# Kernel tuning notes

Hardware: AMD Instinct MI355X
Metric: run time of the kernel (lower is better)

The kernel has to match this reference:

```python
import jax, jax.numpy as jnp
import numpy as np

B, S, E, H = 2, 2048, 512, 8
DH = E // H
SCALE = DH ** -0.5
TEMPERATURE = 1.0
LN_EPS = 1e-5


def setup_inputs() -> dict:
    key = jax.random.key(0)
    ks = jax.random.split(key, 12)
    s = E ** -0.5
    return {
        "q": jax.random.normal(ks[0], (B, S, E), jnp.float32),
        "k": jax.random.normal(ks[1], (B, S, E), jnp.float32),
        "v": jax.random.normal(ks[2], (B, S, E), jnp.float32),
        "Wq": jax.random.normal(ks[3], (E, E), jnp.float32) * s,
        "bq": jnp.zeros((E,), jnp.float32),
        "Wk": jax.random.normal(ks[4], (E, E), jnp.float32) * s,
        "bk": jnp.zeros((E,), jnp.float32),
        "Wv": jax.random.normal(ks[5], (E, E), jnp.float32) * s,
        "bv": jnp.zeros((E,), jnp.float32),
        "Wo": jax.random.normal(ks[6], (E, E), jnp.float32) * s,
        "bo": jnp.zeros((E,), jnp.float32),
        "ln_g": jnp.ones((E,), jnp.float32),
        "ln_b": jnp.zeros((E,), jnp.float32),
    }


def reference(q, k, v, Wq, bq, Wk, bk, Wv, bv, Wo, bo, ln_g, ln_b):
    # QKV projections (nn.Linear: x @ W.T + b)
    qh = (q @ Wq.T + bq).reshape(B, S, H, DH).transpose(0, 2, 1, 3)  # [B,H,S,Dh]
    kh = (k @ Wk.T + bk).reshape(B, S, H, DH).transpose(0, 2, 1, 3)
    vh = (v @ Wv.T + bv).reshape(B, S, H, DH).transpose(0, 2, 1, 3)
    # attention scores [B,H,S,S], scaled then divided by temperature
    scores = jnp.einsum('bhqd,bhkd->bhqk', qh, kh) * (SCALE / TEMPERATURE)
    attn = jax.nn.softmax(scores, axis=-1)
    # dropout is identity in eval mode
    x = jnp.einsum('bhqk,bhkd->bhqd', attn, vh)  # [B,H,S,Dh]
    x = x.transpose(0, 2, 1, 3).reshape(B, S, E)
    # out projection + LayerNorm
    y = x @ Wo.T + bo
    mu = jnp.mean(y, axis=-1, keepdims=True)
    var = jnp.var(y, axis=-1, keepdims=True)
    out = (y - mu) * jax.lax.rsqrt(var + LN_EPS) * ln_g + ln_b
    return out
```

## Files before the change

### kernel.cpp

```cpp
#include <hip/hip_runtime.h>
#include <hip/hip_bf16.h>
#include <stdint.h>

#define B_ 2
#define S_ 2048
#define E_ 512
#define H_ 8
#define DH_ 64
#define BH_ (B_*H_)
#define M_ (B_*S_)

typedef short short8 __attribute__((ext_vector_type(8)));
typedef float f32x4 __attribute__((ext_vector_type(4)));
typedef float f32x16 __attribute__((ext_vector_type(16)));
typedef int int4v __attribute__((ext_vector_type(4)));

#define QSCALE 0.18033688011112042f

#if __has_builtin(__builtin_amdgcn_exp2f)
#define EXP2(x) __builtin_amdgcn_exp2f(x)
#else
#define EXP2(x) exp2f(x)
#endif

__device__ __forceinline__ float asf(uint32_t u) { return __builtin_bit_cast(float, u); }
__device__ __forceinline__ uint32_t asu(float f) { return __builtin_bit_cast(uint32_t, f); }

__device__ __forceinline__ ushort f2bf(float f) {
  uint32_t u = __builtin_bit_cast(uint32_t, f);
  u += 0x7fffu + ((u >> 16) & 1u);
  return (ushort)(u >> 16);
}

__device__ __forceinline__ uint32_t cvtpk(float lo, float hi) {
  uint32_t r;
  asm("v_cvt_pk_bf16_f32 %0, %1, %2" : "=v"(r) : "v"(lo), "v"(hi));
  return r;
}

__device__ __forceinline__ void swap32(uint32_t a, uint32_t b, uint32_t& o0, uint32_t& o1) {
#if __has_builtin(__builtin_amdgcn_permlane32_swap)
  typedef int v2i __attribute__((ext_vector_type(2)));
  v2i r = __builtin_amdgcn_permlane32_swap((int)a, (int)b, false, false);
  o0 = (uint32_t)r.x; o1 = (uint32_t)r.y;
#else
  int laneid = (int)(threadIdx.x & 63);
  uint32_t pa = (uint32_t)__shfl_xor((int)a, 32, 64);
  uint32_t pb = (uint32_t)__shfl_xor((int)b, 32, 64);
  bool hi = laneid >= 32;
  o0 = hi ? pb : a;
  o1 = hi ? b : pa;
#endif
}

__device__ __forceinline__ void gll16(const void* g, void* l) {
  __builtin_amdgcn_global_load_lds((const __attribute__((address_space(1))) void*)g,
                                   (__attribute__((address_space(3))) void*)l,
                                   16, 0, 0);
}

struct CvtArgs {
  const float* s[7];
  ushort* d[7];
  int nq[7];
};

__global__ __launch_bounds__(256) void cvt_kernel(CvtArgs a) {
  int seg = blockIdx.y;
  int i = blockIdx.x * 256 + threadIdx.x;
  if (i >= a.nq[seg]) return;
  float4 v = ((const float4*)a.s[seg])[i];
  ushort4 o;
  o.x = f2bf(v.x); o.y = f2bf(v.y); o.z = f2bf(v.z); o.w = f2bf(v.w);
  ((ushort4*)a.d[seg])[i] = o;
}

template<int EPI>
__global__ __launch_bounds__(256) void gemm_bt(
    const ushort* __restrict__ A0, const ushort* __restrict__ A1, const ushort* __restrict__ A2,
    const ushort* __restrict__ W0, const ushort* __restrict__ W1, const ushort* __restrict__ W2,
    const float* __restrict__ bias0, const float* __restrict__ bias1, const float* __restrict__ bias2,
    ushort* O0, ushort* O1, ushort* O2, float* Yout)
{
  const int K = E_;
  int z = blockIdx.z;
  const ushort* A = (z == 0) ? A0 : ((z == 1) ? A1 : A2);
  const ushort* W = (z == 0) ? W0 : ((z == 1) ? W1 : W2);
  const float* bias = (z == 0) ? bias0 : ((z == 1) ? bias1 : bias2);
  ushort* O = (z == 0) ? O0 : ((z == 1) ? O1 : O2);
  float scale = (EPI == 0 && z == 0) ? QSCALE : 1.0f;

  int n0 = blockIdx.x * 128, m0 = blockIdx.y * 128;
  int tid = threadIdx.x, lane = tid & 63, wid = tid >> 6;
  int wm = wid >> 1, wn = wid & 1;

  __shared__ ushort As[128 * 32];
  __shared__ ushort Bs[128 * 32];

  f32x4 acc[4][4];
#pragma unroll
  for (int i = 0; i < 4; ++i)
#pragma unroll
    for (int j = 0; j < 4; ++j)
      acc[i][j] = (f32x4){0.f, 0.f, 0.f, 0.f};

  for (int kt = 0; kt < K / 32; ++kt) {
    int k0 = kt * 32;
#pragma unroll
    for (int c = 0; c < 2; ++c) {
      int f = c * 256 + tid;
      int r = f >> 2;
      int lc = (f & 3) ^ ((r >> 1) & 3);
      gll16(A + (m0 + r) * K + k0 + lc * 8, (char*)As + (c * 256 + wid * 64) * 16);
    }
#pragma unroll
    for (int c = 0; c < 2; ++c) {
      int f = c * 256 + tid;
      int r = f >> 2;
      int lc = (f & 3) ^ ((r >> 1) & 3);
      gll16(W + (n0 + r) * K + k0 + lc * 8, (char*)Bs + (c * 256 + wid * 64) * 16);
    }
    __syncthreads();

    short8 af[4], bf[4];
#pragma unroll
    for (int fm = 0; fm < 4; ++fm) {
      int r = wm * 64 + fm * 16 + (lane & 15);
      int phys = (lane >> 4) ^ ((r >> 1) & 3);
      af[fm] = *(const short8*)((const char*)As + r * 64 + phys * 16);
    }
#pragma unroll
    for (int fn = 0; fn < 4; ++fn) {
      int r = wn * 64 + fn * 16 + (lane & 15);
      int phys = (lane >> 4) ^ ((r >> 1) & 3);
      bf[fn] = *(const short8*)((const char*)Bs + r * 64 + phys * 16);
    }
#pragma unroll
    for (int fm = 0; fm < 4; ++fm)
#pragma unroll
      for (int fn = 0; fn < 4; ++fn)
        acc[fm][fn] = __builtin_amdgcn_mfma_f32_16x16x32_bf16(af[fm], bf[fn], acc[fm][fn], 0, 0, 0);
    __syncthreads();
  }

#pragma unroll
  for (int fm = 0; fm < 4; ++fm) {
#pragma unroll
    for (int fn = 0; fn < 4; ++fn) {
#pragma unroll
      for (int j = 0; j < 4; ++j) {
        int m = m0 + wm * 64 + fm * 16 + (lane >> 4) * 4 + j;
        int n = n0 + wn * 64 + fn * 16 + (lane & 15);
        float v = (acc[fm][fn][j] + bias[n]) * scale;
        if constexpr (EPI == 0) {
          int b = m >> 11, s = m & (S_ - 1);
          int h = n >> 6, d = n & 63;
          O[((b * H_ + h) * S_ + s) * DH_ + d] = f2bf(v);
        } else {
          Yout[m * E_ + n] = v;
        }
      }
    }
  }
}

__global__ __launch_bounds__(256) void vtrans(const ushort* __restrict__ Vh, ushort* __restrict__ Vt) {
  int bh = blockIdx.y;
  int s0 = blockIdx.x * 64;
  __shared__ ushort t[64][72];
  int tid = threadIdx.x;
  const ushort* src = Vh + ((size_t)bh * S_ + s0) * DH_;
  int r = tid >> 2, c0 = (tid & 3) * 16;
#pragma unroll
  for (int i = 0; i < 2; ++i) {
    short8 v = *(const short8*)(src + r * DH_ + c0 + i * 8);
#pragma unroll
    for (int kx = 0; kx < 8; ++kx) t[r][c0 + i * 8 + kx] = (ushort)v[kx];
  }
  __syncthreads();
  int d = tid >> 2, j0 = (tid & 3) * 16;
  ushort* dst = Vt + ((size_t)bh * DH_ + d) * S_ + s0 + j0;
#pragma unroll
  for (int i = 0; i < 2; ++i) {
    short8 o;
#pragma unroll
    for (int kx = 0; kx < 8; ++kx) o[kx] = (short)t[j0 + i * 8 + kx][d];
    *(short8*)(dst + i * 8) = o;
  }
}

__global__ __launch_bounds__(512, 4) void attn_kernel(const ushort* __restrict__ Qh,
                                                      const ushort* __restrict__ Kh,
                                                      const ushort* __restrict__ Vt,
                                                      ushort* __restrict__ X) {
  int bh = blockIdx.x;
  int q0 = blockIdx.y * 64;
  int tid = threadIdx.x, lane = tid & 63, wid = tid >> 6;
  int wq = wid & 1, wk = wid >> 1;
  int hi = lane >> 5;

  __shared__ ushort lds_[32768];
  char* L = (char*)lds_;

  const ushort* Kg = Kh + (size_t)bh * S_ * DH_;
  const ushort* Vg = Vt + (size_t)bh * DH_ * S_;

  int q = q0 + wq * 32 + (lane & 31);
  const ushort* Qrow = Qh + ((size_t)bh * S_ + q) * DH_;
  short8 qf[4];
#pragma unroll
  for (int ds = 0; ds < 4; ++ds)
    qf[ds] = *(const short8*)(Qrow + ds * 16 + hi * 8);

  f32x16 sacc, oacc[2];
#pragma unroll
  for (int r = 0; r < 16; ++r) { oacc[0][r] = 0.f; oacc[1][r] = 0.f; }
  float m_r = -INFINITY, l_r = 0.f;

  const int NT = 16;

#define STAGE(buf, t)                                                          \
  do {                                                                         \
    int kb = wk * 512 + (t) * 32;                                              \
    char* tb = L + (buf) * 32768 + wk * 8192;                                  \
    if (wq == 0) {                                                             \
      _Pragma("unroll")                                                        \
      for (int kk = 0; kk < 4; ++kk) {                                         \
        int r = kk * 8 + (lane >> 3), c = lane & 7;                            \
        int lc = c ^ (r & 7);                                                  \
        gll16(Kg + (size_t)(kb + r) * DH_ + lc * 8, tb + kk * 1024);           \
      }                                                                        \
    } else {                                                                   \
      _Pragma("unroll")                                                        \
      for (int kk = 0; kk < 4; ++kk) {                                         \
        int rho = kk * 8 + (lane >> 3), c = lane & 7;                          \
        int l2 = c ^ (rho & 7);                                                \
        int d = rho + ((l2 >> 2) << 5), kc = (l2 & 3) * 8;                     \
        gll16(Vg + (size_t)d * S_ + kb + kc, tb + 4096 + kk * 1024);           \
      }                                                                        \
    }                                                                          \
  } while (0)

  STAGE(0, 0);
  __syncthreads();

  for (int t = 0; t < NT; ++t) {
    int cur = t & 1;
    if (t + 1 < NT) STAGE(cur ^ 1, t + 1);

    const char* Kt = L + cur * 32768 + wk * 8192;
    const char* Vtile = Kt + 4096;

#pragma unroll
    for (int r = 0; r < 16; ++r) sacc[r] = 0.f;
    int kl = lane & 31;
    __builtin_amdgcn_s_setprio(1);
#pragma unroll
    for (int ds = 0; ds < 4; ++ds) {
      short8 kf = *(const short8*)(Kt + kl * 128 + (((2 * ds + hi) ^ (kl & 7)) * 16));
      sacc = __builtin_amdgcn_mfma_f32_32x32x16_bf16(kf, qf[ds], sacc, 0, 0, 0);
    }
    __builtin_amdgcn_s_setprio(0);

    float mx = fmaxf(fmaxf(sacc[0], sacc[1]), sacc[2]);
    mx = fmaxf(mx, fmaxf(fmaxf(sacc[3], sacc[4]), sacc[5]));
    mx = fmaxf(mx, fmaxf(fmaxf(sacc[6], sacc[7]), sacc[8]));
    mx = fmaxf(mx, fmaxf(fmaxf(sacc[9], sacc[10]), sacc[11]));
    mx = fmaxf(mx, fmaxf(fmaxf(sacc[12], sacc[13]), sacc[14]));
    mx = fmaxf(mx, sacc[15]);
    bool skip = __all(mx - m_r <= 8.0f);
    if (!skip) {
      uint32_t e0, e1;
      swap32(asu(mx), asu(mx), e0, e1);
      float mnew = fmaxf(m_r, fmaxf(asf(e0), asf(e1)));
      float scf = EXP2(m_r - mnew);
      m_r = mnew;
      l_r *= scf;
#pragma unroll
      for (int dblk = 0; dblk < 2; ++dblk)
#pragma unroll
        for (int r = 0; r < 16; ++r) oacc[dblk][r] *= scf;
    }
    float rs0 = 0.f, rs1 = 0.f;
#pragma unroll
    for (int r = 0; r < 16; r += 2) {
      float p0 = EXP2(sacc[r] - m_r);
      float p1 = EXP2(sacc[r + 1] - m_r);
      sacc[r] = p0; sacc[r + 1] = p1;
      rs0 += p0; rs1 += p1;
    }
    float rs = rs0 + rs1;
    {
      uint32_t e0, e1;
      swap32(asu(rs), asu(rs), e0, e1);
      l_r += asf(e0) + asf(e1);
    }

    uint32_t w[8];
#pragma unroll
    for (int i = 0; i < 8; ++i)
      w[i] = cvtpk(sacc[2 * i], sacc[2 * i + 1]);

    short8 pf[2];
#pragma unroll
    for (int ks = 0; ks < 2; ++ks) {
      uint32_t e01, e45, e23, e67;
      swap32(w[4 * ks + 0], w[4 * ks + 2], e01, e45);
      swap32(w[4 * ks + 1], w[4 * ks + 3], e23, e67);
      int4v iv;
      iv[0] = (int)e01; iv[1] = (int)e23; iv[2] = (int)e45; iv[3] = (int)e67;
      pf[ks] = __builtin_bit_cast(short8, iv);
    }

    __builtin_amdgcn_s_setprio(1);
#pragma unroll
    for (int ks = 0; ks < 2; ++ks) {
      int rho = lane & 31;
#pragma unroll
      for (int dblk = 0; dblk < 2; ++dblk) {
        int lch = dblk * 4 + 2 * ks + hi;
        short8 vf = *(const short8*)(Vtile + rho * 128 + ((lch ^ (rho & 7)) * 16));
        oacc[dblk] = __builtin_amdgcn_mfma_f32_32x32x16_bf16(vf, pf[ks], oacc[dblk], 0, 0, 0);
      }
    }
    __builtin_amdgcn_s_setprio(0);

    __syncthreads();
  }
#undef STAGE

  float* fl = (float*)L;
  if (wk != 0) {
    int pb = ((wk - 1) * 2 + wq) * 2;
#pragma unroll
    for (int dblk = 0; dblk < 2; ++dblk)
#pragma unroll
      for (int r = 0; r < 16; ++r)
        fl[(pb + dblk) * 1024 + r * 64 + lane] = oacc[dblk][r];
    fl[12288 + ((wk - 1) * 2 + wq) * 64 + lane] = m_r;
    fl[12672 + ((wk - 1) * 2 + wq) * 64 + lane] = l_r;
  }
  __syncthreads();
  if (wk == 0) {
    float mm[3], ll[3];
#pragma unroll
    for (int i = 0; i < 3; ++i) {
      mm[i] = fl[12288 + (i * 2 + wq) * 64 + lane];
      ll[i] = fl[12672 + (i * 2 + wq) * 64 + lane];
    }
    float mstar = fmaxf(fmaxf(m_r, mm[0]), fmaxf(mm[1], mm[2]));
    float a0 = EXP2(m_r - mstar);
    float lstar = l_r * a0;
    float aa[3];
#pragma unroll
    for (int i = 0; i < 3; ++i) {
      aa[i] = EXP2(mm[i] - mstar);
      lstar += ll[i] * aa[i];
    }
#pragma unroll
    for (int dblk = 0; dblk < 2; ++dblk)
#pragma unroll
      for (int r = 0; r < 16; ++r) {
        float o = oacc[dblk][r] * a0;
#pragma unroll
        for (int i = 0; i < 3; ++i)
          o += fl[((i * 2 + wq) * 2 + dblk) * 1024 + r * 64 + lane] * aa[i];
        oacc[dblk][r] = o;
      }
    float invl = 1.0f / lstar;
    int b = bh >> 3, h = bh & 7;
    int s = q0 + wq * 32 + (lane & 31);
    ushort* Xrow = X + (size_t)(b * S_ + s) * E_ + h * DH_;
#pragma unroll
    for (int dblk = 0; dblk < 2; ++dblk) {
#pragma unroll
      for (int i = 0; i < 8; ++i) {
        int r0 = 2 * i, r1 = 2 * i + 1;
        float o0 = oacc[dblk][r0] * invl;
        float o1 = oacc[dblk][r1] * invl;
        int d = dblk * 32 + (r0 & 3) + 8 * (r0 >> 2) + 4 * hi;
        *(uint32_t*)(Xrow + d) = cvtpk(o0, o1);
      }
    }
  }
}

__global__ __launch_bounds__(256) void ln_kernel(const float* __restrict__ Y,
                                                 const float* __restrict__ g,
                                                 const float* __restrict__ bta,
                                                 float* __restrict__ out) {
  int tid = threadIdx.x, lane = tid & 63, wid = tid >> 6;
  int row = blockIdx.x * 4 + wid;
  const float* y = Y + (size_t)row * E_;
  float4 v0 = *(const float4*)(y + lane * 8);
  float4 v1 = *(const float4*)(y + lane * 8 + 4);
  float s = v0.x + v0.y + v0.z + v0.w + v1.x + v1.y + v1.z + v1.w;
  float q = v0.x * v0.x + v0.y * v0.y + v0.z * v0.z + v0.w * v0.w +
            v1.x * v1.x + v1.y * v1.y + v1.z * v1.z + v1.w * v1.w;
#pragma unroll
  for (int msk = 1; msk < 64; msk <<= 1) {
    s += __shfl_xor(s, msk);
    q += __shfl_xor(q, msk);
  }
  float mu = s * (1.f / E_);
  float var = q * (1.f / E_) - mu * mu;
  float inv = rsqrtf(var + 1e-5f);
  float4 g0 = *(const float4*)(g + lane * 8);
  float4 g1 = *(const float4*)(g + lane * 8 + 4);
  float4 b0 = *(const float4*)(bta + lane * 8);
  float4 b1 = *(const float4*)(bta + lane * 8 + 4);
  float4 o0, o1;
  o0.x = (v0.x - mu) * inv * g0.x + b0.x;
  o0.y = (v0.y - mu) * inv * g0.y + b0.y;
  o0.z = (v0.z - mu) * inv * g0.z + b0.z;
  o0.w = (v0.w - mu) * inv * g0.w + b0.w;
  o1.x = (v1.x - mu) * inv * g1.x + b1.x;
  o1.y = (v1.y - mu) * inv * g1.y + b1.y;
  o1.z = (v1.z - mu) * inv * g1.z + b1.z;
  o1.w = (v1.w - mu) * inv * g1.w + b1.w;
  float* op = out + (size_t)row * E_;
  *(float4*)(op + lane * 8) = o0;
  *(float4*)(op + lane * 8 + 4) = o1;
}

extern "C" void kernel_launch(void* const* d_in, const int* in_sizes, int n_in,
                              void* d_out, int out_size, void* d_ws, size_t ws_size,
                              hipStream_t stream) {
  const float* q = (const float*)d_in[0];
  const float* k = (const float*)d_in[1];
  const float* v = (const float*)d_in[2];
  const float* Wq = (const float*)d_in[3];
  const float* bq = (const float*)d_in[4];
  const float* Wk = (const float*)d_in[5];
  const float* bk = (const float*)d_in[6];
  const float* Wv = (const float*)d_in[7];
  const float* bv = (const float*)d_in[8];
  const float* Wo = (const float*)d_in[9];
  const float* bo = (const float*)d_in[10];
  const float* ln_g = (const float*)d_in[11];
  const float* ln_b = (const float*)d_in[12];

  char* ws = (char*)d_ws;
  const size_t MB = 1024 * 1024;
  ushort* qb  = (ushort*)(ws + 0 * MB);
  ushort* kb  = (ushort*)(ws + 4 * MB);
  ushort* vb  = (ushort*)(ws + 8 * MB);
  ushort* Wqb = (ushort*)(ws + 12 * MB);
  ushort* Wkb = (ushort*)(ws + 12 * MB + 512 * 1024);
  ushort* Wvb = (ushort*)(ws + 13 * MB);
  ushort* Wob = (ushort*)(ws + 13 * MB + 512 * 1024);
  ushort* Qhb = (ushort*)(ws + 14 * MB);
  ushort* Khb = (ushort*)(ws + 18 * MB);
  ushort* Vhb = (ushort*)(ws + 22 * MB);
  ushort* Vtb = (ushort*)(ws + 26 * MB);
  ushort* Xb  = (ushort*)(ws + 30 * MB);
  float*  Yb  = (float*)(ws + 34 * MB);

  CvtArgs ca;
  ca.s[0] = q;  ca.d[0] = qb;  ca.nq[0] = (B_ * S_ * E_) / 4;
  ca.s[1] = k;  ca.d[1] = kb;  ca.nq[1] = (B_ * S_ * E_) / 4;
  ca.s[2] = v;  ca.d[2] = vb;  ca.nq[2] = (B_ * S_ * E_) / 4;
  ca.s[3] = Wq; ca.d[3] = Wqb; ca.nq[3] = (E_ * E_) / 4;
  ca.s[4] = Wk; ca.d[4] = Wkb; ca.nq[4] = (E_ * E_) / 4;
  ca.s[5] = Wv; ca.d[5] = Wvb; ca.nq[5] = (E_ * E_) / 4;
  ca.s[6] = Wo; ca.d[6] = Wob; ca.nq[6] = (E_ * E_) / 4;

  cvt_kernel<<<dim3(2048, 7), dim3(256), 0, stream>>>(ca);

  gemm_bt<0><<<dim3(4, 32, 3), dim3(256), 0, stream>>>(
      qb, kb, vb, Wqb, Wkb, Wvb, bq, bk, bv, Qhb, Khb, Vhb, (float*)nullptr);

  vtrans<<<dim3(S_ / 64, BH_), dim3(256), 0, stream>>>(Vhb, Vtb);

  attn_kernel<<<dim3(BH_, S_ / 64), dim3(512), 0, stream>>>(Qhb, Khb, Vtb, Xb);

  gemm_bt<1><<<dim3(4, 32, 1), dim3(256), 0, stream>>>(
      Xb, Xb, Xb, Wob, Wob, Wob, bo, bo, bo,
      (ushort*)nullptr, (ushort*)nullptr, (ushort*)nullptr, Yb);

  ln_kernel<<<dim3(M_ / 4), dim3(256), 0, stream>>>(Yb, ln_g, ln_b, (float*)d_out);
}
```

Measured before the change: 78.39 us.

## Load K/V fragments directly from global into registers, drop LDS staging in attention

```diff
diff --git a/kernel.cpp b/kernel.cpp
--- a/kernel.cpp
+++ b/kernel.cpp
@@ -189,78 +189,67 @@
   }
 }
 
-__global__ __launch_bounds__(512, 4) void attn_kernel(const ushort* __restrict__ Qh,
+__global__ __launch_bounds__(256, 3) void attn_kernel(const ushort* __restrict__ Qh,
                                                       const ushort* __restrict__ Kh,
                                                       const ushort* __restrict__ Vt,
                                                       ushort* __restrict__ X) {
-  int bh = blockIdx.x;
-  int q0 = blockIdx.y * 64;
-  int tid = threadIdx.x, lane = tid & 63, wid = tid >> 6;
-  int wq = wid & 1, wk = wid >> 1;
+  int blk = blockIdx.x;
+  int bh = blk >> 6;
+  int q0 = (blk & 63) * 32;
+  int tid = threadIdx.x, lane = tid & 63, wv = tid >> 6;
   int hi = lane >> 5;
-
-  __shared__ ushort lds_[32768];
-  char* L = (char*)lds_;
+  int kl = lane & 31;
+
+  __shared__ float fl[6528];
 
   const ushort* Kg = Kh + (size_t)bh * S_ * DH_;
   const ushort* Vg = Vt + (size_t)bh * DH_ * S_;
 
-  int q = q0 + wq * 32 + (lane & 31);
-  const ushort* Qrow = Qh + ((size_t)bh * S_ + q) * DH_;
-  short8 qf[4];
-#pragma unroll
-  for (int ds = 0; ds < 4; ++ds)
-    qf[ds] = *(const short8*)(Qrow + ds * 16 + hi * 8);
-
-  f32x16 sacc, oacc[2];
-#pragma unroll
-  for (int r = 0; r < 16; ++r) { oacc[0][r] = 0.f; oacc[1][r] = 0.f; }
+  const ushort* Qrow = Qh + ((size_t)bh * S_ + q0 + kl) * DH_ + hi * 8;
+  short8 qf0 = *(const short8*)(Qrow + 0 * 16);
+  short8 qf1 = *(const short8*)(Qrow + 1 * 16);
+  short8 qf2 = *(const short8*)(Qrow + 2 * 16);
+  short8 qf3 = *(const short8*)(Qrow + 3 * 16);
+
+  int kbase = wv * 512;
+  const ushort* Kl = Kg + (size_t)(kbase + kl) * DH_ + hi * 8;
+  const ushort* Vl0 = Vg + (size_t)kl * S_ + kbase + hi * 8;
+  const ushort* Vl1 = Vg + (size_t)(kl + 32) * S_ + kbase + hi * 8;
+
+  f32x16 sacc, oacc0, oacc1;
+#pragma unroll
+  for (int r = 0; r < 16; ++r) { oacc0[r] = 0.f; oacc1[r] = 0.f; }
   float m_r = -INFINITY, l_r = 0.f;
 
   const int NT = 16;
 
-#define STAGE(buf, t)                                                          \
-  do {                                                                         \
-    int kb = wk * 512 + (t) * 32;                                              \
-    char* tb = L + (buf) * 32768 + wk * 8192;                                  \
-    if (wq == 0) {                                                             \
-      _Pragma("unroll")                                                        \
-      for (int kk = 0; kk < 4; ++kk) {                                         \
-        int r = kk * 8 + (lane >> 3), c = lane & 7;                            \
-        int lc = c ^ (r & 7);                                                  \
-        gll16(Kg + (size_t)(kb + r) * DH_ + lc * 8, tb + kk * 1024);           \
-      }                                                                        \
-    } else {                                                                   \
-      _Pragma("unroll")                                                        \
-      for (int kk = 0; kk < 4; ++kk) {                                         \
-        int rho = kk * 8 + (lane >> 3), c = lane & 7;                          \
-        int l2 = c ^ (rho & 7);                                                \
-        int d = rho + ((l2 >> 2) << 5), kc = (l2 & 3) * 8;                     \
-        gll16(Vg + (size_t)d * S_ + kb + kc, tb + 4096 + kk * 1024);           \
-      }                                                                        \
-    }                                                                          \
-  } while (0)
-
-  STAGE(0, 0);
-  __syncthreads();
+  short8 k0 = *(const short8*)(Kl + 0);
+  short8 k1 = *(const short8*)(Kl + 16);
+  short8 k2 = *(const short8*)(Kl + 32);
+  short8 k3 = *(const short8*)(Kl + 48);
 
   for (int t = 0; t < NT; ++t) {
-    int cur = t & 1;
-    if (t + 1 < NT) STAGE(cur ^ 1, t + 1);
-
-    const char* Kt = L + cur * 32768 + wk * 8192;
-    const char* Vtile = Kt + 4096;
+    int tn = (t + 1 < NT) ? t + 1 : t;
+    const ushort* Kn = Kl + (size_t)tn * 32 * DH_;
+    short8 n0 = *(const short8*)(Kn + 0);
+    short8 n1 = *(const short8*)(Kn + 16);
+    short8 n2 = *(const short8*)(Kn + 32);
+    short8 n3 = *(const short8*)(Kn + 48);
 
 #pragma unroll
     for (int r = 0; r < 16; ++r) sacc[r] = 0.f;
-    int kl = lane & 31;
     __builtin_amdgcn_s_setprio(1);
-#pragma unroll
-    for (int ds = 0; ds < 4; ++ds) {
-      short8 kf = *(const short8*)(Kt + kl * 128 + (((2 * ds + hi) ^ (kl & 7)) * 16));
-      sacc = __builtin_amdgcn_mfma_f32_32x32x16_bf16(kf, qf[ds], sacc, 0, 0, 0);
-    }
+    sacc = __builtin_amdgcn_mfma_f32_32x32x16_bf16(k0, qf0, sacc, 0, 0, 0);
+    sacc = __builtin_amdgcn_mfma_f32_32x32x16_bf16(k1, qf1, sacc, 0, 0, 0);
+    sacc = __builtin_amdgcn_mfma_f32_32x32x16_bf16(k2, qf2, sacc, 0, 0, 0);
+    sacc = __builtin_amdgcn_mfma_f32_32x32x16_bf16(k3, qf3, sacc, 0, 0, 0);
     __builtin_amdgcn_s_setprio(0);
+
+    int voff = t * 32;
+    short8 v00 = *(const short8*)(Vl0 + voff);
+    short8 v10 = *(const short8*)(Vl0 + voff + 16);
+    short8 v01 = *(const short8*)(Vl1 + voff);
+    short8 v11 = *(const short8*)(Vl1 + voff + 16);
 
     float mx = fmaxf(fmaxf(sacc[0], sacc[1]), sacc[2]);
     mx = fmaxf(mx, fmaxf(fmaxf(sacc[3], sacc[4]), sacc[5]));
@@ -277,9 +266,7 @@
       m_r = mnew;
       l_r *= scf;
 #pragma unroll
-      for (int dblk = 0; dblk < 2; ++dblk)
-#pragma unroll
-        for (int r = 0; r < 16; ++r) oacc[dblk][r] *= scf;
+      for (int r = 0; r < 16; ++r) { oacc0[r] *= scf; oacc1[r] *= scf; }
     }
     float rs0 = 0.f, rs1 = 0.f;
 #pragma unroll
@@ -313,40 +300,32 @@
     }
 
     __builtin_amdgcn_s_setprio(1);
-#pragma unroll
-    for (int ks = 0; ks < 2; ++ks) {
-      int rho = lane & 31;
-#pragma unroll
-      for (int dblk = 0; dblk < 2; ++dblk) {
-        int lch = dblk * 4 + 2 * ks + hi;
-        short8 vf = *(const short8*)(Vtile + rho * 128 + ((lch ^ (rho & 7)) * 16));
-        oacc[dblk] = __builtin_amdgcn_mfma_f32_32x32x16_bf16(vf, pf[ks], oacc[dblk], 0, 0, 0);
-      }
-    }
+    oacc0 = __builtin_amdgcn_mfma_f32_32x32x16_bf16(v00, pf[0], oacc0, 0, 0, 0);
+    oacc1 = __builtin_amdgcn_mfma_f32_32x32x16_bf16(v01, pf[0], oacc1, 0, 0, 0);
+    oacc0 = __builtin_amdgcn_mfma_f32_32x32x16_bf16(v10, pf[1], oacc0, 0, 0, 0);
+    oacc1 = __builtin_amdgcn_mfma_f32_32x32x16_bf16(v11, pf[1], oacc1, 0, 0, 0);
     __builtin_amdgcn_s_setprio(0);
 
-    __syncthreads();
-  }
-#undef STAGE
-
-  float* fl = (float*)L;
-  if (wk != 0) {
-    int pb = ((wk - 1) * 2 + wq) * 2;
-#pragma unroll
-    for (int dblk = 0; dblk < 2; ++dblk)
-#pragma unroll
-      for (int r = 0; r < 16; ++r)
-        fl[(pb + dblk) * 1024 + r * 64 + lane] = oacc[dblk][r];
-    fl[12288 + ((wk - 1) * 2 + wq) * 64 + lane] = m_r;
-    fl[12672 + ((wk - 1) * 2 + wq) * 64 + lane] = l_r;
+    k0 = n0; k1 = n1; k2 = n2; k3 = n3;
+  }
+
+  if (wv != 0) {
+    int i = wv - 1;
+#pragma unroll
+    for (int r = 0; r < 16; ++r) {
+      fl[(i * 2 + 0) * 1024 + r * 64 + lane] = oacc0[r];
+      fl[(i * 2 + 1) * 1024 + r * 64 + lane] = oacc1[r];
+    }
+    fl[6144 + i * 64 + lane] = m_r;
+    fl[6336 + i * 64 + lane] = l_r;
   }
   __syncthreads();
-  if (wk == 0) {
+  if (wv == 0) {
     float mm[3], ll[3];
 #pragma unroll
     for (int i = 0; i < 3; ++i) {
-      mm[i] = fl[12288 + (i * 2 + wq) * 64 + lane];
-      ll[i] = fl[12672 + (i * 2 + wq) * 64 + lane];
+      mm[i] = fl[6144 + i * 64 + lane];
+      ll[i] = fl[6336 + i * 64 + lane];
     }
     float mstar = fmaxf(fmaxf(m_r, mm[0]), fmaxf(mm[1], mm[2]));
     float a0 = EXP2(m_r - mstar);
@@ -358,29 +337,25 @@
       lstar += ll[i] * aa[i];
     }
 #pragma unroll
-    for (int dblk = 0; dblk < 2; ++dblk)
-#pragma unroll
-      for (int r = 0; r < 16; ++r) {
-        float o = oacc[dblk][r] * a0;
-#pragma unroll
-        for (int i = 0; i < 3; ++i)
-          o += fl[((i * 2 + wq) * 2 + dblk) * 1024 + r * 64 + lane] * aa[i];
-        oacc[dblk][r] = o;
+    for (int r = 0; r < 16; ++r) {
+      float o0 = oacc0[r] * a0, o1 = oacc1[r] * a0;
+#pragma unroll
+      for (int i = 0; i < 3; ++i) {
+        o0 += fl[(i * 2 + 0) * 1024 + r * 64 + lane] * aa[i];
+        o1 += fl[(i * 2 + 1) * 1024 + r * 64 + lane] * aa[i];
       }
+      oacc0[r] = o0; oacc1[r] = o1;
+    }
     float invl = 1.0f / lstar;
     int b = bh >> 3, h = bh & 7;
-    int s = q0 + wq * 32 + (lane & 31);
+    int s = q0 + kl;
     ushort* Xrow = X + (size_t)(b * S_ + s) * E_ + h * DH_;
 #pragma unroll
-    for (int dblk = 0; dblk < 2; ++dblk) {
-#pragma unroll
-      for (int i = 0; i < 8; ++i) {
-        int r0 = 2 * i, r1 = 2 * i + 1;
-        float o0 = oacc[dblk][r0] * invl;
-        float o1 = oacc[dblk][r1] * invl;
-        int d = dblk * 32 + (r0 & 3) + 8 * (r0 >> 2) + 4 * hi;
-        *(uint32_t*)(Xrow + d) = cvtpk(o0, o1);
-      }
+    for (int i = 0; i < 8; ++i) {
+      int r0 = 2 * i, r1 = 2 * i + 1;
+      int d = (r0 & 3) + 8 * (r0 >> 2) + 4 * hi;
+      *(uint32_t*)(Xrow + d)      = cvtpk(oacc0[r0] * invl, oacc0[r1] * invl);
+      *(uint32_t*)(Xrow + 32 + d) = cvtpk(oacc1[r0] * invl, oacc1[r1] * invl);
     }
   }
 }
@@ -472,7 +447,7 @@
 
   vtrans<<<dim3(S_ / 64, BH_), dim3(256), 0, stream>>>(Vhb, Vtb);
 
-  attn_kernel<<<dim3(BH_, S_ / 64), dim3(512), 0, stream>>>(Qhb, Khb, Vtb, Xb);
+  attn_kernel<<<dim3(BH_ * 64), dim3(256), 0, stream>>>(Qhb, Khb, Vtb, Xb);
 
   gemm_bt<1><<<dim3(4, 32, 1), dim3(256), 0, stream>>>(
       Xb, Xb, Xb, Wob, Wob, Wob, bo, bo, bo,
```

Measured after the change: 110.9 us. +41.5%, slower.
